# Kernel optimization log

Hardware: AMD Instinct MI355X
Metric: run time of the kernel (lower is better)

The kernel has to match this reference:

```python
import jax, jax.numpy as jnp
import numpy as np

LN_EPS = 1e-12

def setup_inputs() -> dict:
    key = jax.random.key(0)
    k1, k2 = jax.random.split(key)
    batch, seq_len, hidden, conv_size = 32, 2048, 512, 64
    input_tensor = jax.random.normal(k1, (batch, seq_len, hidden), dtype=jnp.float32)
    conv_weight = jax.random.normal(k2, (1, conv_size, hidden), dtype=jnp.float32) * 0.02
    gamma = jnp.ones((hidden,), dtype=jnp.float32)
    beta = jnp.zeros((hidden,), dtype=jnp.float32)
    return {"input_tensor": input_tensor, "conv_weight": conv_weight, "gamma": gamma, "beta": beta}

def reference(input_tensor, conv_weight, gamma, beta):
    # input_tensor: [B, S, H]; conv_weight: [1, K, H] (K << S)
    seq_len = input_tensor.shape[1]
    conv_size = conv_weight.shape[1]
    # FFT-based circular depthwise convolution along the sequence axis
    x_f = jnp.fft.rfft(input_tensor, axis=1, norm='ortho')            # [B, S//2+1, H] complex
    w_pad = jnp.pad(conv_weight, ((0, 0), (0, seq_len - conv_size), (0, 0)))  # zero-pad filter to S
    w_f = jnp.fft.rfft(w_pad, axis=1, norm='ortho')                   # [1, S//2+1, H]
    y = jnp.fft.irfft(x_f * w_f, n=seq_len, axis=1, norm='ortho')     # [B, S, H]
    # dropout is identity at inference; residual + LayerNorm(eps=1e-12)
    h = y + input_tensor
    mean = jnp.mean(h, axis=-1, keepdims=True)
    var = jnp.mean(jnp.square(h - mean), axis=-1, keepdims=True)
    return gamma * (h - mean) * jax.lax.rsqrt(var + LN_EPS) + beta
```

## Files before the change

### kernel.cpp

```cpp
#include <hip/hip_runtime.h>

#define S_LEN 2048
#define HDIM  512
#define KSZ   64
#define S_T   128
#define PH    16
#define INV_SQRT_S 0.02209708691207961f

struct Smem {
    float  lh[PH][HDIM];
    float2 part[PH][33];
    float2 stats[PH];
};

__device__ __forceinline__ void lds_barrier() {
    asm volatile("s_waitcnt lgkmcnt(0)\n\ts_barrier" ::: "memory");
}

template <int OFF>
__device__ __forceinline__ void conv_phase(const float* __restrict__ xb, int sbase, int h,
                                           const float (&wr)[KSZ], float (&xw)[KSZ],
                                           float (&xp)[PH], float (&hv)[PH], Smem* sm)
{
#pragma unroll
    for (int j = 0; j < PH; ++j) {
        const float xcur = xp[j];
        xp[j] = xb[((sbase + j + PH) & (S_LEN - 1)) * HDIM + h];

        float y0 = 0.f, y1 = 0.f, y2 = 0.f, y3 = 0.f;
#pragma unroll
        for (int k = 1; k <= KSZ - 7; k += 4) {
            y0 = fmaf(wr[k],     xw[(OFF + j - k)     & 63], y0);
            y1 = fmaf(wr[k + 1], xw[(OFF + j - k - 1) & 63], y1);
            y2 = fmaf(wr[k + 2], xw[(OFF + j - k - 2) & 63], y2);
            y3 = fmaf(wr[k + 3], xw[(OFF + j - k - 3) & 63], y3);
        }
        y0 = fmaf(wr[61], xw[(OFF + j - 61) & 63], y0);
        y1 = fmaf(wr[62], xw[(OFF + j - 62) & 63], y1);
        y2 = fmaf(wr[63], xw[(OFF + j - 63) & 63], y2);

        const float hval = fmaf(INV_SQRT_S, fmaf(wr[0], xcur, (y0 + y1) + (y2 + y3)), xcur);
        xw[(OFF + j) & 63] = xcur;
        hv[j] = hval;
        sm->lh[j][h] = hval;
    }
}

__device__ __forceinline__ void ln_phase(int sbase, int h, const float (&hv)[PH],
                                         float gm, float bt, float* __restrict__ ob, Smem* sm)
{
    lds_barrier();

    const int r = h >> 5, c = h & 31;
    float s1 = 0.f, q1 = 0.f;
#pragma unroll
    for (int m = 0; m < 16; ++m) {
        const float v = sm->lh[r][c + (m << 5)];
        s1 += v;
        q1 = fmaf(v, v, q1);
    }
    sm->part[r][c] = make_float2(s1, q1);
    lds_barrier();

    if (h < 64) {
        const int rr = h >> 2, q = h & 3;
        float ts = 0.f, tq = 0.f;
#pragma unroll
        for (int i = 0; i < 8; ++i) {
            const float2 p = sm->part[rr][q * 8 + i];
            ts += p.x; tq += p.y;
        }
        ts += __shfl_xor(ts, 1, 64); tq += __shfl_xor(tq, 1, 64);
        ts += __shfl_xor(ts, 2, 64); tq += __shfl_xor(tq, 2, 64);
        if (q == 0) {
            const float mean = ts * (1.0f / 512.0f);
            const float var  = fmaf(tq, 1.0f / 512.0f, -mean * mean);
            sm->stats[rr] = make_float2(mean, rsqrtf(var + 1e-12f));
        }
    }
    lds_barrier();

#pragma unroll
    for (int j = 0; j < PH; ++j) {
        const float2 st = sm->stats[j];
        ob[(sbase + j) * HDIM + h] = fmaf((hv[j] - st.x) * st.y, gm, bt);
    }
}

__global__ __launch_bounds__(512, 2)
void fconv_ln(const float* __restrict__ x, const float* __restrict__ w,
              const float* __restrict__ gamma, const float* __restrict__ beta,
              float* __restrict__ out)
{
    __shared__ Smem sm;
    const int h  = threadIdx.x;
    const int b  = blockIdx.x >> 4;
    const int s0 = (blockIdx.x & 15) * S_T;

    const float* xb = x   + (size_t)b * S_LEN * HDIM;
    float*       ob = out + (size_t)b * S_LEN * HDIM;

    float wr[KSZ];
#pragma unroll
    for (int k = 0; k < KSZ; ++k) wr[k] = w[k * HDIM + h];
    const float gm = gamma[h], bt = beta[h];

    float xw[KSZ];
#pragma unroll
    for (int d = 1; d < KSZ; ++d)
        xw[KSZ - d] = xb[((s0 - d) & (S_LEN - 1)) * HDIM + h];
    xw[0] = 0.f;

    float xp[PH], hv[PH];
#pragma unroll
    for (int j = 0; j < PH; ++j) xp[j] = xb[(s0 + j) * HDIM + h];

    for (int grp = 0; grp < S_T / 64; ++grp) {
        const int base = s0 + grp * 64;
        conv_phase<0 >(xb, base +  0, h, wr, xw, xp, hv, &sm); ln_phase(base +  0, h, hv, gm, bt, ob, &sm);
        conv_phase<16>(xb, base + 16, h, wr, xw, xp, hv, &sm); ln_phase(base + 16, h, hv, gm, bt, ob, &sm);
        conv_phase<32>(xb, base + 32, h, wr, xw, xp, hv, &sm); ln_phase(base + 32, h, hv, gm, bt, ob, &sm);
        conv_phase<48>(xb, base + 48, h, wr, xw, xp, hv, &sm); ln_phase(base + 48, h, hv, gm, bt, ob, &sm);
    }
}

extern "C" void kernel_launch(void* const* d_in, const int* in_sizes, int n_in,
                              void* d_out, int out_size, void* d_ws, size_t ws_size,
                              hipStream_t stream) {
    const float* x  = (const float*)d_in[0];
    const float* w  = (const float*)d_in[1];
    const float* g  = (const float*)d_in[2];
    const float* b  = (const float*)d_in[3];
    float* o        = (float*)d_out;

    (void)in_sizes; (void)n_in; (void)out_size; (void)d_ws; (void)ws_size;
    fconv_ln<<<dim3(32 * (S_LEN / S_T)), dim3(HDIM), 0, stream>>>(x, w, g, b, o);
}
```

Before: 263.9 us.

## Stream filter weights from memory and use an 80-entry register ring buffer

```diff
diff --git a/kernel.cpp b/kernel.cpp
--- a/kernel.cpp
+++ b/kernel.cpp
@@ -5,6 +5,7 @@
 #define KSZ   64
 #define S_T   128
 #define PH    16
+#define RING  80
 #define INV_SQRT_S 0.02209708691207961f
 
 struct Smem {
@@ -17,30 +18,58 @@
     asm volatile("s_waitcnt lgkmcnt(0)\n\ts_barrier" ::: "memory");
 }
 
-template <int OFF>
-__device__ __forceinline__ void conv_phase(const float* __restrict__ xb, int sbase, int h,
-                                           const float (&wr)[KSZ], float (&xw)[KSZ],
-                                           float (&xp)[PH], float (&hv)[PH], Smem* sm)
+template <int OFF, bool STAGE>
+__device__ __forceinline__ void conv_phase(const float* __restrict__ xb,
+                                           const float* __restrict__ wp,
+                                           int sbase, int h,
+                                           float (&ring)[RING], float (&xpa)[8],
+                                           float (&hv)[PH], Smem* sm)
 {
 #pragma unroll
+    for (int j = 0; j < 8; ++j) ring[(OFF + j) % RING] = xpa[j];
+
+    if (STAGE) {
+#pragma unroll
+        for (int j = 0; j < 8; ++j)
+            xpa[j] = xb[((sbase + PH + j) & (S_LEN - 1)) * HDIM + h];
+    }
+
+#pragma unroll
+    for (int j = 0; j < PH; ++j) hv[j] = 0.f;
+
+    float wv[3][4];
+#pragma unroll
+    for (int u = 0; u < 4; ++u) wv[0][u] = wp[u * HDIM];
+#pragma unroll
+    for (int u = 0; u < 4; ++u) wv[1][u] = wp[(4 + u) * HDIM];
+
+#pragma unroll
+    for (int kb = 0; kb < 16; ++kb) {
+        if (kb < 14) {
+#pragma unroll
+            for (int u = 0; u < 4; ++u)
+                wv[(kb + 2) % 3][u] = wp[((kb + 2) * 4 + u) * HDIM];
+        }
+#pragma unroll
+        for (int u = 0; u < 4; ++u) {
+            const int k = kb * 4 + u;
+            const float wk = wv[kb % 3][u];
+#pragma unroll
+            for (int j = 0; j < PH; ++j)
+                hv[j] = fmaf(wk, ring[(OFF + j - k + RING) % RING], hv[j]);
+        }
+    }
+
+    if (STAGE) {
+#pragma unroll
+        for (int j = 0; j < 8; ++j)
+            ring[(OFF + 24 + j) % RING] =
+                xb[((sbase + 24 + j) & (S_LEN - 1)) * HDIM + h];
+    }
+
+#pragma unroll
     for (int j = 0; j < PH; ++j) {
-        const float xcur = xp[j];
-        xp[j] = xb[((sbase + j + PH) & (S_LEN - 1)) * HDIM + h];
-
-        float y0 = 0.f, y1 = 0.f, y2 = 0.f, y3 = 0.f;
-#pragma unroll
-        for (int k = 1; k <= KSZ - 7; k += 4) {
-            y0 = fmaf(wr[k],     xw[(OFF + j - k)     & 63], y0);
-            y1 = fmaf(wr[k + 1], xw[(OFF + j - k - 1) & 63], y1);
-            y2 = fmaf(wr[k + 2], xw[(OFF + j - k - 2) & 63], y2);
-            y3 = fmaf(wr[k + 3], xw[(OFF + j - k - 3) & 63], y3);
-        }
-        y0 = fmaf(wr[61], xw[(OFF + j - 61) & 63], y0);
-        y1 = fmaf(wr[62], xw[(OFF + j - 62) & 63], y1);
-        y2 = fmaf(wr[63], xw[(OFF + j - 63) & 63], y2);
-
-        const float hval = fmaf(INV_SQRT_S, fmaf(wr[0], xcur, (y0 + y1) + (y2 + y3)), xcur);
-        xw[(OFF + j) & 63] = xcur;
+        const float hval = fmaf(INV_SQRT_S, hv[j], ring[(OFF + j) % RING]);
         hv[j] = hval;
         sm->lh[j][h] = hval;
     }
@@ -99,29 +128,31 @@
 
     const float* xb = x   + (size_t)b * S_LEN * HDIM;
     float*       ob = out + (size_t)b * S_LEN * HDIM;
-
-    float wr[KSZ];
-#pragma unroll
-    for (int k = 0; k < KSZ; ++k) wr[k] = w[k * HDIM + h];
+    const float* wp = w + h;
     const float gm = gamma[h], bt = beta[h];
 
-    float xw[KSZ];
+    float ring[RING];
 #pragma unroll
-    for (int d = 1; d < KSZ; ++d)
-        xw[KSZ - d] = xb[((s0 - d) & (S_LEN - 1)) * HDIM + h];
-    xw[0] = 0.f;
+    for (int d = 1; d <= 63; ++d)
+        ring[64 - d] = xb[((s0 - d) & (S_LEN - 1)) * HDIM + h];
+    ring[0] = 0.f;
+#pragma unroll
+    for (int j = 0; j < 8; ++j)
+        ring[72 + j] = xb[(s0 + 8 + j) * HDIM + h];
+    float xpa[8];
+#pragma unroll
+    for (int j = 0; j < 8; ++j)
+        xpa[j] = xb[(s0 + j) * HDIM + h];
 
-    float xp[PH], hv[PH];
-#pragma unroll
-    for (int j = 0; j < PH; ++j) xp[j] = xb[(s0 + j) * HDIM + h];
-
-    for (int grp = 0; grp < S_T / 64; ++grp) {
-        const int base = s0 + grp * 64;
-        conv_phase<0 >(xb, base +  0, h, wr, xw, xp, hv, &sm); ln_phase(base +  0, h, hv, gm, bt, ob, &sm);
-        conv_phase<16>(xb, base + 16, h, wr, xw, xp, hv, &sm); ln_phase(base + 16, h, hv, gm, bt, ob, &sm);
-        conv_phase<32>(xb, base + 32, h, wr, xw, xp, hv, &sm); ln_phase(base + 32, h, hv, gm, bt, ob, &sm);
-        conv_phase<48>(xb, base + 48, h, wr, xw, xp, hv, &sm); ln_phase(base + 48, h, hv, gm, bt, ob, &sm);
-    }
+    float hv[PH];
+    conv_phase<64, true >(xb, wp, s0 +   0, h, ring, xpa, hv, &sm); ln_phase(s0 +   0, h, hv, gm, bt, ob, &sm);
+    conv_phase< 0, true >(xb, wp, s0 +  16, h, ring, xpa, hv, &sm); ln_phase(s0 +  16, h, hv, gm, bt, ob, &sm);
+    conv_phase<16, true >(xb, wp, s0 +  32, h, ring, xpa, hv, &sm); ln_phase(s0 +  32, h, hv, gm, bt, ob, &sm);
+    conv_phase<32, true >(xb, wp, s0 +  48, h, ring, xpa, hv, &sm); ln_phase(s0 +  48, h, hv, gm, bt, ob, &sm);
+    conv_phase<48, true >(xb, wp, s0 +  64, h, ring, xpa, hv, &sm); ln_phase(s0 +  64, h, hv, gm, bt, ob, &sm);
+    conv_phase<64, true >(xb, wp, s0 +  80, h, ring, xpa, hv, &sm); ln_phase(s0 +  80, h, hv, gm, bt, ob, &sm);
+    conv_phase< 0, true >(xb, wp, s0 +  96, h, ring, xpa, hv, &sm); ln_phase(s0 +  96, h, hv, gm, bt, ob, &sm);
+    conv_phase<16, false>(xb, wp, s0 + 112, h, ring, xpa, hv, &sm); ln_phase(s0 + 112, h, hv, gm, bt, ob, &sm);
 }
 
 extern "C" void kernel_launch(void* const* d_in, const int* in_sizes, int n_in,
```

Result: slower. 284.0 us (+7.6%).

## Per-wave LayerNorm rows with double-buffered LDS and higher occupancy

Applied to the files above, without the earlier changes.

```diff
diff --git a/kernel.cpp b/kernel.cpp
--- a/kernel.cpp
+++ b/kernel.cpp
@@ -8,24 +8,22 @@
 #define INV_SQRT_S 0.02209708691207961f
 
 struct Smem {
-    float  lh[PH][HDIM];
-    float2 part[PH][33];
-    float2 stats[PH];
+    float lh[2][PH][HDIM];
 };
 
 __device__ __forceinline__ void lds_barrier() {
     asm volatile("s_waitcnt lgkmcnt(0)\n\ts_barrier" ::: "memory");
 }
 
-template <int OFF>
+template <int OFF, int BUF>
 __device__ __forceinline__ void conv_phase(const float* __restrict__ xb, int sbase, int h,
                                            const float (&wr)[KSZ], float (&xw)[KSZ],
-                                           float (&xp)[PH], float (&hv)[PH], Smem* sm)
+                                           float (&xp)[8], Smem* sm)
 {
 #pragma unroll
     for (int j = 0; j < PH; ++j) {
-        const float xcur = xp[j];
-        xp[j] = xb[((sbase + j + PH) & (S_LEN - 1)) * HDIM + h];
+        const float xcur = xp[j & 7];
+        xp[j & 7] = xb[((sbase + j + 8) & (S_LEN - 1)) * HDIM + h];
 
         float y0 = 0.f, y1 = 0.f, y2 = 0.f, y3 = 0.f;
 #pragma unroll
@@ -41,59 +39,60 @@
 
         const float hval = fmaf(INV_SQRT_S, fmaf(wr[0], xcur, (y0 + y1) + (y2 + y3)), xcur);
         xw[(OFF + j) & 63] = xcur;
-        hv[j] = hval;
-        sm->lh[j][h] = hval;
+        sm->lh[BUF][j][h] = hval;
     }
 }
 
-__device__ __forceinline__ void ln_phase(int sbase, int h, const float (&hv)[PH],
-                                         float gm, float bt, float* __restrict__ ob, Smem* sm)
+template <int BUF>
+__device__ __forceinline__ void ln_phase(int sbase, int lane, int wv,
+                                         const float* __restrict__ gamma,
+                                         const float* __restrict__ beta,
+                                         float* __restrict__ ob, Smem* sm)
 {
     lds_barrier();
 
-    const int r = h >> 5, c = h & 31;
-    float s1 = 0.f, q1 = 0.f;
+    float gm[8], bt[8];
 #pragma unroll
-    for (int m = 0; m < 16; ++m) {
-        const float v = sm->lh[r][c + (m << 5)];
-        s1 += v;
-        q1 = fmaf(v, v, q1);
+    for (int m = 0; m < 8; ++m) {
+        gm[m] = gamma[lane + 64 * m];
+        bt[m] = beta [lane + 64 * m];
     }
-    sm->part[r][c] = make_float2(s1, q1);
-    lds_barrier();
-
-    if (h < 64) {
-        const int rr = h >> 2, q = h & 3;
-        float ts = 0.f, tq = 0.f;
-#pragma unroll
-        for (int i = 0; i < 8; ++i) {
-            const float2 p = sm->part[rr][q * 8 + i];
-            ts += p.x; tq += p.y;
-        }
-        ts += __shfl_xor(ts, 1, 64); tq += __shfl_xor(tq, 1, 64);
-        ts += __shfl_xor(ts, 2, 64); tq += __shfl_xor(tq, 2, 64);
-        if (q == 0) {
-            const float mean = ts * (1.0f / 512.0f);
-            const float var  = fmaf(tq, 1.0f / 512.0f, -mean * mean);
-            sm->stats[rr] = make_float2(mean, rsqrtf(var + 1e-12f));
-        }
-    }
-    lds_barrier();
 
 #pragma unroll
-    for (int j = 0; j < PH; ++j) {
-        const float2 st = sm->stats[j];
-        ob[(sbase + j) * HDIM + h] = fmaf((hv[j] - st.x) * st.y, gm, bt);
+    for (int rr = 0; rr < 2; ++rr) {
+        const int row = wv * 2 + rr;
+        float v[8];
+        float s = 0.f, q = 0.f;
+#pragma unroll
+        for (int m = 0; m < 8; ++m) {
+            v[m] = sm->lh[BUF][row][lane + 64 * m];
+            s += v[m];
+            q = fmaf(v[m], v[m], q);
+        }
+#pragma unroll
+        for (int d = 1; d < 64; d <<= 1) {
+            s += __shfl_xor(s, d, 64);
+            q += __shfl_xor(q, d, 64);
+        }
+        const float mean = s * (1.0f / 512.0f);
+        const float rstd = rsqrtf(fmaf(q, 1.0f / 512.0f, -mean * mean) + 1e-12f);
+
+        float* op = ob + (size_t)(sbase + row) * HDIM + lane;
+#pragma unroll
+        for (int m = 0; m < 8; ++m)
+            op[64 * m] = fmaf(v[m] - mean, rstd * gm[m], bt[m]);
     }
 }
 
-__global__ __launch_bounds__(512, 2)
+__global__ __launch_bounds__(512, 4)
 void fconv_ln(const float* __restrict__ x, const float* __restrict__ w,
               const float* __restrict__ gamma, const float* __restrict__ beta,
               float* __restrict__ out)
 {
     __shared__ Smem sm;
-    const int h  = threadIdx.x;
+    const int h    = threadIdx.x;
+    const int lane = h & 63;
+    const int wv   = h >> 6;
     const int b  = blockIdx.x >> 4;
     const int s0 = (blockIdx.x & 15) * S_T;
 
@@ -103,7 +102,6 @@
     float wr[KSZ];
 #pragma unroll
     for (int k = 0; k < KSZ; ++k) wr[k] = w[k * HDIM + h];
-    const float gm = gamma[h], bt = beta[h];
 
     float xw[KSZ];
 #pragma unroll
@@ -111,16 +109,16 @@
         xw[KSZ - d] = xb[((s0 - d) & (S_LEN - 1)) * HDIM + h];
     xw[0] = 0.f;
 
-    float xp[PH], hv[PH];
+    float xp[8];
 #pragma unroll
-    for (int j = 0; j < PH; ++j) xp[j] = xb[(s0 + j) * HDIM + h];
+    for (int j = 0; j < 8; ++j) xp[j] = xb[(s0 + j) * HDIM + h];
 
     for (int grp = 0; grp < S_T / 64; ++grp) {
         const int base = s0 + grp * 64;
-        conv_phase<0 >(xb, base +  0, h, wr, xw, xp, hv, &sm); ln_phase(base +  0, h, hv, gm, bt, ob, &sm);
-        conv_phase<16>(xb, base + 16, h, wr, xw, xp, hv, &sm); ln_phase(base + 16, h, hv, gm, bt, ob, &sm);
-        conv_phase<32>(xb, base + 32, h, wr, xw, xp, hv, &sm); ln_phase(base + 32, h, hv, gm, bt, ob, &sm);
-        conv_phase<48>(xb, base + 48, h, wr, xw, xp, hv, &sm); ln_phase(base + 48, h, hv, gm, bt, ob, &sm);
+        conv_phase< 0, 0>(xb, base +  0, h, wr, xw, xp, &sm); ln_phase<0>(base +  0, lane, wv, gamma, beta, ob, &sm);
+        conv_phase<16, 1>(xb, base + 16, h, wr, xw, xp, &sm); ln_phase<1>(base + 16, lane, wv, gamma, beta, ob, &sm);
+        conv_phase<32, 0>(xb, base + 32, h, wr, xw, xp, &sm); ln_phase<0>(base + 32, lane, wv, gamma, beta, ob, &sm);
+        conv_phase<48, 1>(xb, base + 48, h, wr, xw, xp, &sm); ln_phase<1>(base + 48, lane, wv, gamma, beta, ob, &sm);
     }
 }
 
```

Measured after the change: 667.7 us. 2.53x slower.
